# Kernel optimization log

Measured on AMD Instinct MI355X. Metric: run time of the kernel, lower is better.

Reference implementation:

```python
import jax, jax.numpy as jnp
import numpy as np

B, T, C, H = 4, 2048, 1024, 16
D = C // H  # head dim = 64


def setup_inputs() -> dict:
    key = jax.random.key(0)
    ks = jax.random.split(key, 5)
    s = 1.0 / np.sqrt(C)
    return {
        "x": jax.random.normal(ks[0], (B, T, C), dtype=jnp.float32),
        "Wq": jax.random.normal(ks[1], (C, C), dtype=jnp.float32) * s,
        "bq": jnp.zeros((C,), dtype=jnp.float32),
        "Wk": jax.random.normal(ks[2], (C, C), dtype=jnp.float32) * s,
        "bk": jnp.zeros((C,), dtype=jnp.float32),
        "Wv": jax.random.normal(ks[3], (C, C), dtype=jnp.float32) * s,
        "bv": jnp.zeros((C,), dtype=jnp.float32),
        "Wp": jax.random.normal(ks[4], (C, C), dtype=jnp.float32) * s,
        "bp": jnp.zeros((C,), dtype=jnp.float32),
    }


def reference(x, Wq, bq, Wk, bk, Wv, bv, Wp, bp):
    Bb, Tt, Cc = x.shape
    # QKV projections (torch Linear: y = x @ W.T + b)
    q = (x @ Wq.T + bq).reshape(Bb, Tt, H, D).transpose(0, 2, 1, 3)  # [B,H,T,D]
    k = (x @ Wk.T + bk).reshape(Bb, Tt, H, D).transpose(0, 2, 1, 3)
    v = (x @ Wv.T + bv).reshape(Bb, Tt, H, D).transpose(0, 2, 1, 3)
    att = jnp.einsum("bhqd,bhkd->bhqk", q, k) / jnp.sqrt(jnp.float32(D))
    causal = jnp.tril(jnp.ones((Tt, Tt), dtype=bool))
    att = jnp.where(causal[None, None], att, -jnp.inf)
    att = jax.nn.softmax(att, axis=-1)
    y = jnp.einsum("bhqk,bhkd->bhqd", att, v)  # [B,H,T,D]
    y = y.transpose(0, 2, 1, 3).reshape(Bb, Tt, Cc)
    return y @ Wp.T + bp
```

## Files before the change

### kernel.cpp

```cpp
#include <hip/hip_runtime.h>

typedef unsigned short u16;
typedef unsigned int u32;

typedef __attribute__((ext_vector_type(4))) float f32x4;
typedef __attribute__((ext_vector_type(8))) short bf16x8;


__device__ inline u16 f2b(float f) {
  union { float f; u32 u; } x; x.f = f;
  u32 u = x.u;
  u32 r = (u + 0x7fffu + ((u >> 16) & 1u)) >> 16;
  return (u16)r;
}

__device__ inline u32 cvtpk(float lo, float hi) {
  u32 r;
  asm("v_cvt_pk_bf16_f32 %0, %1, %2" : "=v"(r) : "v"(lo), "v"(hi));
  return r;
}

__device__ inline void gload_lds16(const void* g, void* l) {
  __builtin_amdgcn_global_load_lds(
      (const __attribute__((address_space(1))) u32*)g,
      (__attribute__((address_space(3))) u32*)l, 16, 0, 0);
}


__global__ __launch_bounds__(256) void cvt_all(const float* __restrict__ x,
                                               const float* __restrict__ w0,
                                               const float* __restrict__ w1,
                                               const float* __restrict__ w2,
                                               const float* __restrict__ w3,
                                               u16* __restrict__ xo,
                                               u16* __restrict__ wo) {
  int b = blockIdx.x;
  const float* s;
  u16* d;
  int i;
  if (b < 8192) {
    s = x; d = xo; i = b * 256 + threadIdx.x;
  } else {
    int m = (b - 8192) >> 10;
    s = (m == 0) ? w0 : (m == 1) ? w1 : (m == 2) ? w2 : w3;
    d = wo + (size_t)m * 1048576;
    i = ((b - 8192) & 1023) * 256 + threadIdx.x;
  }
  float4 v = ((const float4*)s)[i];
  ushort4 o;
  o.x = f2b(v.x); o.y = f2b(v.y); o.z = f2b(v.z); o.w = f2b(v.w);
  ((ushort4*)d)[i] = o;
}


__global__ __launch_bounds__(256) void gemm_qkv(const u16* __restrict__ A,
                                                const u16* __restrict__ W,
                                                const float* __restrict__ bq,
                                                const float* __restrict__ bk,
                                                const float* __restrict__ bv,
                                                u16* __restrict__ outQ,
                                                u16* __restrict__ outK,
                                                u16* __restrict__ outVt,
                                                float qscale) {
  __shared__ u16 sA[128 * 32];
  __shared__ u16 sB[128 * 32];

  const int K = 1024;
  const int t = threadIdx.x;
  const int lane = t & 63;
  const int w = t >> 6;
  const int wr = w >> 1, wc = w & 1;
  const int lr = lane & 15, lg = lane >> 4;

  int bid = blockIdx.y * 24 + blockIdx.x;
  int swz = (bid & 7) * 192 + (bid >> 3);
  const int mBase = (swz / 24) * 128;
  const int nBase = (swz % 24) * 128;

  f32x4 zero = {0.f, 0.f, 0.f, 0.f};
  f32x4 acc[4][4];
#pragma unroll
  for (int i = 0; i < 4; ++i)
#pragma unroll
    for (int j = 0; j < 4; ++j) acc[i][j] = zero;

  const int rA = t >> 2;
  const int cA = (t & 3) * 8;

  for (int k0 = 0; k0 < K; k0 += 32) {
#pragma unroll
    for (int i = 0; i < 2; ++i) {
      gload_lds16(A + (size_t)(mBase + i * 64 + rA) * K + k0 + cA,
                  &sA[i * 2048 + t * 8]);
      gload_lds16(W + (size_t)(nBase + i * 64 + rA) * K + k0 + cA,
                  &sB[i * 2048 + t * 8]);
    }
    __syncthreads();

    bf16x8 af[4], bf[4];
#pragma unroll
    for (int i = 0; i < 4; ++i)
      af[i] = *(const bf16x8*)&sA[(wr * 64 + i * 16 + lr) * 32 + lg * 8];
#pragma unroll
    for (int j = 0; j < 4; ++j)
      bf[j] = *(const bf16x8*)&sB[(wc * 64 + j * 16 + lr) * 32 + lg * 8];

#pragma unroll
    for (int i = 0; i < 4; ++i)
#pragma unroll
      for (int j = 0; j < 4; ++j)
        acc[i][j] = __builtin_amdgcn_mfma_f32_16x16x32_bf16(af[i], bf[j],
                                                            acc[i][j], 0, 0, 0);
    __syncthreads();
  }

  const int mode = nBase >> 10;
  const float* bias = (mode == 0) ? bq : (mode == 1) ? bk : bv;

#pragma unroll
  for (int i = 0; i < 4; ++i) {
    int row = mBase + wr * 64 + i * 16 + lg * 4;
    int b = row >> 11, tp = row & 2047;
#pragma unroll
    for (int j = 0; j < 4; ++j) {
      int col = nBase + wc * 64 + j * 16 + lr;
      int ncol = col & 1023;
      int h = ncol >> 6, dd = ncol & 63;
      float bv_ = bias[ncol];
      size_t bhOff = (size_t)(b * 16 + h) * 262144;
      if (mode == 2) {
        ushort4 o;
        o.x = f2b(acc[i][j][0] + bv_);
        o.y = f2b(acc[i][j][1] + bv_);
        o.z = f2b(acc[i][j][2] + bv_);
        o.w = f2b(acc[i][j][3] + bv_);
        *(ushort4*)((char*)outVt + bhOff + (tp >> 6) * 8192 + dd * 128 +
                    ((((tp & 63) >> 3) << 4) ^ ((dd & 7) << 4)) +
                    (tp & 7) * 2) = o;
      } else if (mode == 0) {
#pragma unroll
        for (int r = 0; r < 4; ++r)
          outQ[(((size_t)(b * 16 + h) * 2048) + tp + r) * 64 + dd] =
              f2b((acc[i][j][r] + bv_) * qscale);
      } else {
#pragma unroll
        for (int r = 0; r < 4; ++r) {
          int tt = tp + r;
          *(u16*)((char*)outK + bhOff + (tt >> 6) * 8192 + (tt & 63) * 128 +
                  (((dd >> 3) << 4) ^ ((tt & 7) << 4)) + (dd & 7) * 2) =
              f2b(acc[i][j][r] + bv_);
        }
      }
    }
  }
}


__global__ __launch_bounds__(256) void gemm_proj(const u16* __restrict__ A,
                                                 const u16* __restrict__ W,
                                                 const float* __restrict__ bias,
                                                 float* __restrict__ outF) {
  __shared__ u16 sA[128 * 32];
  __shared__ u16 sB[128 * 32];

  const int K = 1024, N = 1024;
  const int t = threadIdx.x;
  const int lane = t & 63;
  const int w = t >> 6;
  const int wr = w >> 1, wc = w & 1;
  const int lr = lane & 15, lg = lane >> 4;

  int bid = blockIdx.y * 8 + blockIdx.x;
  int swz = (bid & 7) * 64 + (bid >> 3);
  const int mBase = (swz >> 3) * 128;
  const int nBase = (swz & 7) * 128;

  f32x4 zero = {0.f, 0.f, 0.f, 0.f};
  f32x4 acc[4][4];
#pragma unroll
  for (int i = 0; i < 4; ++i)
#pragma unroll
    for (int j = 0; j < 4; ++j) acc[i][j] = zero;

  const int rA = t >> 2;
  const int cA = (t & 3) * 8;

  for (int k0 = 0; k0 < K; k0 += 32) {
#pragma unroll
    for (int i = 0; i < 2; ++i) {
      gload_lds16(A + (size_t)(mBase + i * 64 + rA) * K + k0 + cA,
                  &sA[i * 2048 + t * 8]);
      gload_lds16(W + (size_t)(nBase + i * 64 + rA) * K + k0 + cA,
                  &sB[i * 2048 + t * 8]);
    }
    __syncthreads();

    bf16x8 af[4], bf[4];
#pragma unroll
    for (int i = 0; i < 4; ++i)
      af[i] = *(const bf16x8*)&sA[(wr * 64 + i * 16 + lr) * 32 + lg * 8];
#pragma unroll
    for (int j = 0; j < 4; ++j)
      bf[j] = *(const bf16x8*)&sB[(wc * 64 + j * 16 + lr) * 32 + lg * 8];

#pragma unroll
    for (int i = 0; i < 4; ++i)
#pragma unroll
      for (int j = 0; j < 4; ++j)
        acc[i][j] = __builtin_amdgcn_mfma_f32_16x16x32_bf16(af[i], bf[j],
                                                            acc[i][j], 0, 0, 0);
    __syncthreads();
  }

#pragma unroll
  for (int i = 0; i < 4; ++i) {
    int row = mBase + wr * 64 + i * 16 + lg * 4;
#pragma unroll
    for (int j = 0; j < 4; ++j) {
      int col = nBase + wc * 64 + j * 16 + lr;
      float bv = bias[col];
#pragma unroll
      for (int r = 0; r < 4; ++r)
        outF[(size_t)(row + r) * N + col] = acc[i][j][r] + bv;
    }
  }
}


__global__ __launch_bounds__(512) void attn_fwd(const u16* __restrict__ qg,
                                                const u16* __restrict__ kswz,
                                                const u16* __restrict__ vswz,
                                                u16* __restrict__ yg) {
  __shared__ u16 sK[2][64 * 64];
  __shared__ u16 sVt[2][64 * 64];

  const int t = threadIdx.x;
  const int lane = t & 63;
  const int w = t >> 6;
  const int lr = lane & 15, lg = lane >> 4;

  int bid0 = blockIdx.y * 8 + blockIdx.x;
  int swzb = (bid0 & 7) * 64 + (bid0 >> 3);
  const int bh = swzb >> 3;
  const int pair = swzb & 7;

  const char* kgb = (const char*)kswz + (size_t)bh * 262144;
  const char* vgb = (const char*)vswz + (size_t)bh * 262144;
  const u16* qb = qg + (size_t)bh * 131072;

  gload_lds16(kgb + t * 16, (char*)&sK[0][0] + t * 16);
  gload_lds16(vgb + t * 16, (char*)&sVt[0][0] + t * 16);

  f32x4 zero = {0.f, 0.f, 0.f, 0.f};
  const int b = bh >> 4, h = bh & 15;
  int tc = 0;

  for (int half = 0; half < 2; ++half) {
    const int qt = half ? pair : 15 - pair;
    const int nkt = 2 * qt + 2;
    const int wq0 = qt * 128 + w * 16;
    const int qrow = wq0 + lr;

    bf16x8 qf[2];
#pragma unroll
    for (int kk = 0; kk < 2; ++kk)
      qf[kk] = *(const bf16x8*)(qb + (size_t)qrow * 64 + kk * 32 + lg * 8);

    f32x4 accO[4];
#pragma unroll
    for (int n = 0; n < 4; ++n) accO[n] = zero;
    float mrun = -1e30f, lrun = 0.f;

    for (int kt = 0; kt < nkt; ++kt, ++tc) {
      const int cur = tc & 1;
      __syncthreads();

      int nextT = (kt + 1 < nkt) ? kt + 1 : (half == 0 ? 0 : -1);
      if (nextT >= 0) {
        gload_lds16(kgb + nextT * 8192 + t * 16,
                    (char*)&sK[cur ^ 1][0] + t * 16);
        gload_lds16(vgb + nextT * 8192 + t * 16,
                    (char*)&sVt[cur ^ 1][0] + t * 16);
      }

      const char* kb_ = (const char*)&sK[cur][0];
      const char* vb_ = (const char*)&sVt[cur][0];

      f32x4 s[4];
      __builtin_amdgcn_s_setprio(1);
#pragma unroll
      for (int n = 0; n < 4; ++n) {
        f32x4 a = zero;
#pragma unroll
        for (int kk = 0; kk < 2; ++kk) {
          bf16x8 kf = *(const bf16x8*)(kb_ + (n * 16 + lr) * 128 +
                                       ((kk * 64 + lg * 16) ^ ((lr & 7) << 4)));
          a = __builtin_amdgcn_mfma_f32_16x16x32_bf16(kf, qf[kk], a, 0, 0, 0);
        }
        s[n] = a;
      }
      __builtin_amdgcn_s_setprio(0);

      if (kt * 64 + 63 > wq0) {
#pragma unroll
        for (int n = 0; n < 4; ++n) {
          int key0 = kt * 64 + n * 16 + lg * 4;
#pragma unroll
          for (int r = 0; r < 4; ++r)
            s[n][r] = (key0 + r <= qrow) ? s[n][r] : -1e30f;
        }
      }

      float pmax = -1e30f;
#pragma unroll
      for (int n = 0; n < 4; ++n)
        pmax = fmaxf(pmax, fmaxf(fmaxf(s[n][0], s[n][1]), fmaxf(s[n][2], s[n][3])));
      pmax = fmaxf(pmax, __shfl_xor(pmax, 16));
      pmax = fmaxf(pmax, __shfl_xor(pmax, 32));

      const bool full = __any(pmax > mrun + 8.f);
      float mnew = full ? fmaxf(mrun, pmax) : mrun;
      float corr = full ? exp2f(mrun - mnew) : 1.f;
      mrun = mnew;

      float psum = 0.f;
      u32 pk[4][2];
#pragma unroll
      for (int n = 0; n < 4; ++n) {
        float p0 = exp2f(s[n][0] - mnew);
        float p1 = exp2f(s[n][1] - mnew);
        float p2 = exp2f(s[n][2] - mnew);
        float p3 = exp2f(s[n][3] - mnew);
        psum += (p0 + p1) + (p2 + p3);
        pk[n][0] = cvtpk(p0, p1);
        pk[n][1] = cvtpk(p2, p3);
      }
      psum += __shfl_xor(psum, 16);
      psum += __shfl_xor(psum, 32);

      if (full) {
        lrun = lrun * corr + psum;
        float c4[4];
#pragma unroll
        for (int r = 0; r < 4; ++r) c4[r] = __shfl(corr, lg * 4 + r);
#pragma unroll
        for (int n = 0; n < 4; ++n)
#pragma unroll
          for (int r = 0; r < 4; ++r) accO[n][r] *= c4[r];
      } else {
        lrun += psum;
      }

      const bool hi = (lg >> 1) & 1;
#pragma unroll
      for (int kk = 0; kk < 2; ++kk) {
        u32 g[4];
#pragma unroll
        for (int r = 0; r < 4; ++r) {
          const int rh = r >> 1, rl = r & 1;
          u32 give = ((lg & 1) ^ rh) ? pk[2 * kk + 1][rl] : pk[2 * kk][rl];
          int srcLane = ((lg & 1) * 2 + ((lg >> 1) ^ rh)) * 16 + lr;
          g[r] = (u32)__shfl((int)give, srcLane);
        }
        union { u32 u[4]; bf16x8 v; } pu;
        pu.u[0] = hi ? g[2] : g[0];
        pu.u[1] = hi ? g[3] : g[1];
        pu.u[2] = hi ? g[0] : g[2];
        pu.u[3] = hi ? g[1] : g[3];
        bf16x8 pf = pu.v;
        __builtin_amdgcn_s_setprio(1);
#pragma unroll
        for (int n = 0; n < 4; ++n) {
          bf16x8 vf = *(const bf16x8*)(vb_ + (n * 16 + lr) * 128 +
                                       ((kk * 64 + lg * 16) ^ ((lr & 7) << 4)));
          accO[n] = __builtin_amdgcn_mfma_f32_16x16x32_bf16(pf, vf, accO[n], 0, 0, 0);
        }
        __builtin_amdgcn_s_setprio(0);
      }
    }

#pragma unroll
    for (int r = 0; r < 4; ++r) {
      float linv = 1.f / __shfl(lrun, lg * 4 + r);
      int trow = qt * 128 + w * 16 + lg * 4 + r;
      size_t rowOff = ((size_t)b * 2048 + trow) * 1024 + h * 64;
#pragma unroll
      for (int n = 0; n < 4; ++n)
        yg[rowOff + n * 16 + lr] = f2b(accO[n][r] * linv);
    }
  }
}


extern "C" void kernel_launch(void* const* d_in, const int* in_sizes, int n_in,
                              void* d_out, int out_size, void* d_ws, size_t ws_size,
                              hipStream_t stream) {
  const float* x  = (const float*)d_in[0];
  const float* Wq = (const float*)d_in[1];
  const float* bq = (const float*)d_in[2];
  const float* Wk = (const float*)d_in[3];
  const float* bk = (const float*)d_in[4];
  const float* Wv = (const float*)d_in[5];
  const float* bv = (const float*)d_in[6];
  const float* Wp = (const float*)d_in[7];
  const float* bp = (const float*)d_in[8];
  float* out = (float*)d_out;

  char* ws = (char*)d_ws;
  u16* xb  = (u16*)(ws);
  u16* wqb = (u16*)(ws + (16u << 20));
  u16* wpb = (u16*)(ws + (22u << 20));
  u16* qb  = (u16*)(ws + (24u << 20));
  u16* kb  = (u16*)(ws + (40u << 20));
  u16* vtb = (u16*)(ws + (56u << 20));
  u16* yb  = (u16*)(ws + (72u << 20));

  const float SCL = 0.18033688011112042f;

  cvt_all<<<12288, 256, 0, stream>>>(x, Wq, Wk, Wv, Wp, xb, wqb);

  gemm_qkv<<<dim3(24, 64), 256, 0, stream>>>(xb, wqb, bq, bk, bv,
                                             qb, kb, vtb, SCL);

  attn_fwd<<<dim3(8, 64), 512, 0, stream>>>(qb, kb, vtb, yb);

  gemm_proj<<<dim3(8, 64), 256, 0, stream>>>(yb, wpb, bp, out);
}
```

Before: 196.9 us.

## Software-pipeline attention: overlap next tile's QK softmax with current PV

The attention inner loop is restructured so the QK^T and softmax for key tile kt+1 are issued alongside the PV MFMAs for tile kt. K/V shared memory goes from double to triple buffering, with two tiles preloaded up front. The accumulator rescale is deferred until after each PV step. The aim is to hide softmax ALU/exp latency and LDS reads behind matrix work, at the cost of more LDS, more registers for the extra P fragments, and extra buffer-rotation logic between the two query halves.

```diff
diff --git a/kernel.cpp b/kernel.cpp
--- a/kernel.cpp
+++ b/kernel.cpp
@@ -231,13 +231,14 @@
                                                 const u16* __restrict__ kswz,
                                                 const u16* __restrict__ vswz,
                                                 u16* __restrict__ yg) {
-  __shared__ u16 sK[2][64 * 64];
-  __shared__ u16 sVt[2][64 * 64];
+  __shared__ u16 sK[3][64 * 64];
+  __shared__ u16 sVt[3][64 * 64];
 
   const int t = threadIdx.x;
   const int lane = t & 63;
   const int w = t >> 6;
   const int lr = lane & 15, lg = lane >> 4;
+  const int xk = (lr & 7) << 4;
 
   int bid0 = blockIdx.y * 8 + blockIdx.x;
   int swzb = (bid0 & 7) * 64 + (bid0 >> 3);
@@ -248,16 +249,22 @@
   const char* vgb = (const char*)vswz + (size_t)bh * 262144;
   const u16* qb = qg + (size_t)bh * 131072;
 
-  gload_lds16(kgb + t * 16, (char*)&sK[0][0] + t * 16);
-  gload_lds16(vgb + t * 16, (char*)&sVt[0][0] + t * 16);
+  char* sKb = (char*)&sK[0][0];
+  char* sVb = (char*)&sVt[0][0];
+
+  gload_lds16(kgb + t * 16, sKb + t * 16);
+  gload_lds16(vgb + t * 16, sVb + t * 16);
+  gload_lds16(kgb + 8192 + t * 16, sKb + 8192 + t * 16);
+  gload_lds16(vgb + 8192 + t * 16, sVb + 8192 + t * 16);
+  __syncthreads();
 
   f32x4 zero = {0.f, 0.f, 0.f, 0.f};
   const int b = bh >> 4, h = bh & 15;
-  int tc = 0;
+  int c0 = 0, c1 = 1, c2 = 2;
 
   for (int half = 0; half < 2; ++half) {
     const int qt = half ? pair : 15 - pair;
-    const int nkt = 2 * qt + 2;
+    const int n = 2 * qt + 2;
     const int wq0 = qt * 128 + w * 16;
     const int qrow = wq0 + lr;
 
@@ -268,89 +275,69 @@
 
     f32x4 accO[4];
 #pragma unroll
-    for (int n = 0; n < 4; ++n) accO[n] = zero;
+    for (int nn = 0; nn < 4; ++nn) accO[nn] = zero;
     float mrun = -1e30f, lrun = 0.f;
-
-    for (int kt = 0; kt < nkt; ++kt, ++tc) {
-      const int cur = tc & 1;
-      __syncthreads();
-
-      int nextT = (kt + 1 < nkt) ? kt + 1 : (half == 0 ? 0 : -1);
-      if (nextT >= 0) {
-        gload_lds16(kgb + nextT * 8192 + t * 16,
-                    (char*)&sK[cur ^ 1][0] + t * 16);
-        gload_lds16(vgb + nextT * 8192 + t * 16,
-                    (char*)&sVt[cur ^ 1][0] + t * 16);
-      }
-
-      const char* kb_ = (const char*)&sK[cur][0];
-      const char* vb_ = (const char*)&sVt[cur][0];
-
+    u32 pkA[4][2], pkB[4][2];
+
+    auto qksm = [&](int kts, int cb, u32 (&pkO)[4][2], float& corr,
+                    bool& full) {
+      const char* kb_ = sKb + cb * 8192;
       f32x4 s[4];
       __builtin_amdgcn_s_setprio(1);
 #pragma unroll
-      for (int n = 0; n < 4; ++n) {
+      for (int nn = 0; nn < 4; ++nn) {
         f32x4 a = zero;
 #pragma unroll
         for (int kk = 0; kk < 2; ++kk) {
-          bf16x8 kf = *(const bf16x8*)(kb_ + (n * 16 + lr) * 128 +
-                                       ((kk * 64 + lg * 16) ^ ((lr & 7) << 4)));
+          bf16x8 kf = *(const bf16x8*)(kb_ + (nn * 16 + lr) * 128 +
+                                       ((kk * 64 + lg * 16) ^ xk));
           a = __builtin_amdgcn_mfma_f32_16x16x32_bf16(kf, qf[kk], a, 0, 0, 0);
         }
-        s[n] = a;
+        s[nn] = a;
       }
       __builtin_amdgcn_s_setprio(0);
 
-      if (kt * 64 + 63 > wq0) {
-#pragma unroll
-        for (int n = 0; n < 4; ++n) {
-          int key0 = kt * 64 + n * 16 + lg * 4;
+      if (kts * 64 + 63 > wq0) {
+#pragma unroll
+        for (int nn = 0; nn < 4; ++nn) {
+          int key0 = kts * 64 + nn * 16 + lg * 4;
 #pragma unroll
           for (int r = 0; r < 4; ++r)
-            s[n][r] = (key0 + r <= qrow) ? s[n][r] : -1e30f;
+            s[nn][r] = (key0 + r <= qrow) ? s[nn][r] : -1e30f;
         }
       }
 
       float pmax = -1e30f;
 #pragma unroll
-      for (int n = 0; n < 4; ++n)
-        pmax = fmaxf(pmax, fmaxf(fmaxf(s[n][0], s[n][1]), fmaxf(s[n][2], s[n][3])));
+      for (int nn = 0; nn < 4; ++nn)
+        pmax = fmaxf(pmax,
+                     fmaxf(fmaxf(s[nn][0], s[nn][1]), fmaxf(s[nn][2], s[nn][3])));
       pmax = fmaxf(pmax, __shfl_xor(pmax, 16));
       pmax = fmaxf(pmax, __shfl_xor(pmax, 32));
 
-      const bool full = __any(pmax > mrun + 8.f);
+      full = __any(pmax > mrun + 8.f);
       float mnew = full ? fmaxf(mrun, pmax) : mrun;
-      float corr = full ? exp2f(mrun - mnew) : 1.f;
+      corr = full ? exp2f(mrun - mnew) : 1.f;
       mrun = mnew;
 
       float psum = 0.f;
-      u32 pk[4][2];
-#pragma unroll
-      for (int n = 0; n < 4; ++n) {
-        float p0 = exp2f(s[n][0] - mnew);
-        float p1 = exp2f(s[n][1] - mnew);
-        float p2 = exp2f(s[n][2] - mnew);
-        float p3 = exp2f(s[n][3] - mnew);
+#pragma unroll
+      for (int nn = 0; nn < 4; ++nn) {
+        float p0 = exp2f(s[nn][0] - mnew);
+        float p1 = exp2f(s[nn][1] - mnew);
+        float p2 = exp2f(s[nn][2] - mnew);
+        float p3 = exp2f(s[nn][3] - mnew);
         psum += (p0 + p1) + (p2 + p3);
-        pk[n][0] = cvtpk(p0, p1);
-        pk[n][1] = cvtpk(p2, p3);
+        pkO[nn][0] = cvtpk(p0, p1);
+        pkO[nn][1] = cvtpk(p2, p3);
       }
       psum += __shfl_xor(psum, 16);
       psum += __shfl_xor(psum, 32);
-
-      if (full) {
-        lrun = lrun * corr + psum;
-        float c4[4];
-#pragma unroll
-        for (int r = 0; r < 4; ++r) c4[r] = __shfl(corr, lg * 4 + r);
-#pragma unroll
-        for (int n = 0; n < 4; ++n)
-#pragma unroll
-          for (int r = 0; r < 4; ++r) accO[n][r] *= c4[r];
-      } else {
-        lrun += psum;
-      }
-
+      lrun = full ? (lrun * corr + psum) : (lrun + psum);
+    };
+
+    auto pv = [&](int cb, u32 (&pkI)[4][2]) {
+      const char* vb_ = sVb + cb * 8192;
       const bool hi = (lg >> 1) & 1;
 #pragma unroll
       for (int kk = 0; kk < 2; ++kk) {
@@ -358,7 +345,7 @@
 #pragma unroll
         for (int r = 0; r < 4; ++r) {
           const int rh = r >> 1, rl = r & 1;
-          u32 give = ((lg & 1) ^ rh) ? pk[2 * kk + 1][rl] : pk[2 * kk][rl];
+          u32 give = ((lg & 1) ^ rh) ? pkI[2 * kk + 1][rl] : pkI[2 * kk][rl];
           int srcLane = ((lg & 1) * 2 + ((lg >> 1) ^ rh)) * 16 + lr;
           g[r] = (u32)__shfl((int)give, srcLane);
         }
@@ -370,14 +357,51 @@
         bf16x8 pf = pu.v;
         __builtin_amdgcn_s_setprio(1);
 #pragma unroll
-        for (int n = 0; n < 4; ++n) {
-          bf16x8 vf = *(const bf16x8*)(vb_ + (n * 16 + lr) * 128 +
-                                       ((kk * 64 + lg * 16) ^ ((lr & 7) << 4)));
-          accO[n] = __builtin_amdgcn_mfma_f32_16x16x32_bf16(pf, vf, accO[n], 0, 0, 0);
+        for (int nn = 0; nn < 4; ++nn) {
+          bf16x8 vf = *(const bf16x8*)(vb_ + (nn * 16 + lr) * 128 +
+                                       ((kk * 64 + lg * 16) ^ xk));
+          accO[nn] = __builtin_amdgcn_mfma_f32_16x16x32_bf16(pf, vf, accO[nn],
+                                                             0, 0, 0);
         }
         __builtin_amdgcn_s_setprio(0);
       }
-    }
+    };
+
+    float corr;
+    bool full;
+    qksm(0, c0, pkA, corr, full);
+
+    for (int kt = 0; kt < n - 1; ++kt) {
+      __syncthreads();
+
+      int nxt = kt + 2;
+      int koff = (nxt < n) ? nxt * 8192 : ((half == 0) ? 0 : -1);
+      if (koff >= 0) {
+        gload_lds16(kgb + koff + t * 16, sKb + c2 * 8192 + t * 16);
+        gload_lds16(vgb + koff + t * 16, sVb + c2 * 8192 + t * 16);
+      }
+
+      qksm(kt + 1, c1, pkB, corr, full);
+      pv(c0, pkA);
+
+      if (full) {
+        float c4[4];
+#pragma unroll
+        for (int r = 0; r < 4; ++r) c4[r] = __shfl(corr, lg * 4 + r);
+#pragma unroll
+        for (int nn = 0; nn < 4; ++nn)
+#pragma unroll
+          for (int r = 0; r < 4; ++r) accO[nn][r] *= c4[r];
+      }
+#pragma unroll
+      for (int nn = 0; nn < 4; ++nn) {
+        pkA[nn][0] = pkB[nn][0];
+        pkA[nn][1] = pkB[nn][1];
+      }
+      int tmp = c0; c0 = c1; c1 = c2; c2 = tmp;
+    }
+
+    pv(c0, pkA);
 
 #pragma unroll
     for (int r = 0; r < 4; ++r) {
@@ -385,8 +409,15 @@
       int trow = qt * 128 + w * 16 + lg * 4 + r;
       size_t rowOff = ((size_t)b * 2048 + trow) * 1024 + h * 64;
 #pragma unroll
-      for (int n = 0; n < 4; ++n)
-        yg[rowOff + n * 16 + lr] = f2b(accO[n][r] * linv);
+      for (int nn = 0; nn < 4; ++nn)
+        yg[rowOff + nn * 16 + lr] = f2b(accO[nn][r] * linv);
+    }
+
+    if (half == 0) {
+      __syncthreads();
+      gload_lds16(kgb + 8192 + t * 16, sKb + c2 * 8192 + t * 16);
+      gload_lds16(vgb + 8192 + t * 16, sVb + c2 * 8192 + t * 16);
+      int tmp = c0; c0 = c1; c1 = c2; c2 = tmp;
     }
   }
 }
```

Measured after the change: 200.6 us. About the same (+1.9%).
